# Kernel optimization log

Measured on AMD Instinct MI355X. Metric: run time of the kernel, lower is better.

The kernel has to match this reference:

```python
import jax, jax.numpy as jnp
import numpy as np

B, P, Q, D_IN, H, DR = 16, 4096, 512, 512, 256, 256


def setup_inputs() -> dict:
    key = jax.random.key(0)
    ks = jax.random.split(key, 6)
    passage = jax.random.normal(ks[0], (B, P, D_IN), dtype=jnp.float32)
    question = jax.random.normal(ks[1], (B, Q, D_IN), dtype=jnp.float32)
    rep = jax.random.normal(ks[2], (B, Q, DR), dtype=jnp.float32)
    rep_p = jax.random.normal(ks[3], (B, P, DR), dtype=jnp.float32)
    p_mask = jnp.zeros((B, P), dtype=bool)  # True = padding position
    q_mask = jnp.zeros((B, Q), dtype=bool)
    # xavier-uniform-like init for U weight, stored as [in, out]
    limit = float(np.sqrt(6.0 / (D_IN + H)))
    W = jax.random.uniform(ks[4], (D_IN, H), dtype=jnp.float32, minval=-limit, maxval=limit)
    D = jnp.ones((1, H), dtype=jnp.float32)
    return {"passage": passage, "p_mask": p_mask, "question": question,
            "q_mask": q_mask, "rep": rep, "rep_p": rep_p, "W": W, "D": D,
            "is_training": 0}


def reference(passage, p_mask, question, q_mask, rep, rep_p, W, D, is_training):
    # inference path (is_training falsy): no dropout
    Up = jax.nn.relu(passage @ W)              # [B, P, H]
    Uq = jax.nn.relu(question @ W) * D         # [B, Q, H], scaled by diagonal D
    scores = jnp.einsum('bph,bqh->bpq', Up, Uq)  # [B, P, Q]
    # question -> passage direction (rep_p is not None)
    scores_T = jnp.where(p_mask[:, None, :], -jnp.inf, scores.transpose(0, 2, 1))  # [B, Q, P]
    alpha_p = jax.nn.softmax(scores_T, axis=-1)
    output_q = jnp.einsum('bqp,bpd->bqd', alpha_p, rep_p)  # [B, Q, DR]
    # passage -> question direction
    scores_m = jnp.where(q_mask[:, None, :], -jnp.inf, scores)  # [B, P, Q]
    alpha = jax.nn.softmax(scores_m, axis=-1)
    output = jnp.einsum('bpq,bqd->bpd', alpha, rep)  # [B, P, DR]
    return (output, output_q)
```

## Files before the change

### kernel.cpp

```cpp
#include <hip/hip_runtime.h>


typedef float  f32x4   __attribute__((ext_vector_type(4)));
typedef float  float4v __attribute__((ext_vector_type(4)));
typedef short  short8v __attribute__((ext_vector_type(8)));
typedef unsigned short us4 __attribute__((ext_vector_type(4)));
typedef unsigned short us8v __attribute__((ext_vector_type(8)));

#define MFMA16(a,b,c) __builtin_amdgcn_mfma_f32_16x16x32_bf16((a),(b),(c),0,0,0)

__device__ __forceinline__ unsigned short f2bf(float f) {
  unsigned int u = __builtin_bit_cast(unsigned int, f);
  u += 0x7FFFu + ((u >> 16) & 1u);
  return (unsigned short)(u >> 16);
}
__device__ __forceinline__ float bf2f(unsigned short h) {
  unsigned int u = (unsigned int)h << 16;
  return __builtin_bit_cast(float, u);
}
__device__ __forceinline__ void split2(float v, unsigned short& h, unsigned short& l) {
  h = f2bf(v);
  l = f2bf(v - bf2f(h));
}
__device__ __forceinline__ unsigned short enc16(float a, float cm) {
  float x = (a - cm + 20.f) * 3276.8f + 0.5f;
  x = fminf(fmaxf(x, 0.f), 65535.f);
  return (unsigned short)x;
}

__global__ __launch_bounds__(256) void transpose_all(
    const float* __restrict__ W, const float* __restrict__ rep,
    const float* __restrict__ rep_p,
    unsigned short* __restrict__ Wth, unsigned short* __restrict__ Wtl,
    unsigned short* __restrict__ repT, unsigned short* __restrict__ repTp)
{
  __shared__ float lTf[64][65];
  const int blk = blockIdx.x;
  const float* src; unsigned short* dst; unsigned short* dstl = nullptr;
  int srows; size_t r0, c0;
  if (blk < 4096) {
    int b = blk >> 8, tb = blk & 255;
    src = rep_p + (size_t)b * 4096 * 256;
    dst = repTp + (size_t)b * 256 * 4096;
    srows = 4096; r0 = (size_t)(tb >> 2) * 64; c0 = (size_t)(tb & 3) * 64;
  } else if (blk < 4608) {
    int rel = blk - 4096; int b = rel >> 5, tb = rel & 31;
    src = rep + (size_t)b * 512 * 256;
    dst = repT + (size_t)b * 256 * 512;
    srows = 512; r0 = (size_t)(tb >> 2) * 64; c0 = (size_t)(tb & 3) * 64;
  } else {
    int rel = blk - 4608;
    src = W; dst = Wth; dstl = Wtl;
    srows = 512; r0 = (size_t)(rel >> 2) * 64; c0 = (size_t)(rel & 3) * 64;
  }
  const int t = threadIdx.x;
#pragma unroll
  for (int j = 0; j < 4; ++j) {
    int idx = j * 256 + t;
    int r = idx >> 4, c4 = (idx & 15) * 4;
    float4v v = *(const float4v*)&src[(r0 + (size_t)r) * 256 + c0 + c4];
    lTf[r][c4 + 0] = v[0]; lTf[r][c4 + 1] = v[1];
    lTf[r][c4 + 2] = v[2]; lTf[r][c4 + 3] = v[3];
  }
  __syncthreads();
#pragma unroll
  for (int j = 0; j < 4; ++j) {
    int idx = j * 256 + t;
    int dr = idx >> 4, p4 = (idx & 15) * 4;
    size_t o = (c0 + (size_t)dr) * (size_t)srows + r0 + p4;
    if (!dstl) {
      us4 oh;
#pragma unroll
      for (int e = 0; e < 4; ++e) oh[e] = f2bf(lTf[p4 + e][dr]);
      *(us4*)&dst[o] = oh;
    } else {
      us4 oh, ol;
#pragma unroll
      for (int e = 0; e < 4; ++e) {
        unsigned short h, l; split2(lTf[p4 + e][dr], h, l);
        oh[e] = h; ol[e] = l;
      }
      *(us4*)&dst[o] = oh;
      *(us4*)&dstl[o] = ol;
    }
  }
}

template<int APPLY_D>
__global__ __launch_bounds__(256) void ugemm_kernel(
    const float* __restrict__ X,
    const unsigned short* __restrict__ Wth, const unsigned short* __restrict__ Wtl,
    const float* __restrict__ Dv,
    unsigned short* __restrict__ Uh, unsigned short* __restrict__ Ul)
{
  __shared__ unsigned short lAh[64 * 40], lAl[64 * 40];
  __shared__ unsigned short lBh[256 * 40], lBl[256 * 40];
  const int t = threadIdx.x;
  const int w = t >> 6, l = t & 63;
  const int l15 = l & 15, lg = l >> 4, kr = lg * 8;
  const size_t m0 = (size_t)blockIdx.x * 64;
  f32x4 acc[4][4] = {};
  for (int k0 = 0; k0 < 512; k0 += 32) {
    __syncthreads();
    {
      int row = t >> 2, c = (t & 3) * 8;
      const float* src = X + (m0 + row) * 512 + k0 + c;
      float4v v0 = *(const float4v*)src;
      float4v v1 = *(const float4v*)(src + 4);
      short8v ph, pl;
#pragma unroll
      for (int e = 0; e < 4; ++e) {
        unsigned short h, lo;
        split2(v0[e], h, lo); ph[e] = (short)h; pl[e] = (short)lo;
        split2(v1[e], h, lo); ph[4 + e] = (short)h; pl[4 + e] = (short)lo;
      }
      *(short8v*)&lAh[row * 40 + c] = ph;
      *(short8v*)&lAl[row * 40 + c] = pl;
    }
#pragma unroll
    for (int j = 0; j < 4; ++j) {
      int idx = j * 256 + t;
      int row = idx >> 2, c = (idx & 3) * 8;
      size_t g = (size_t)row * 512 + k0 + c;
      *(short8v*)&lBh[row * 40 + c] = *(const short8v*)&Wth[g];
      *(short8v*)&lBl[row * 40 + c] = *(const short8v*)&Wtl[g];
    }
    __syncthreads();
    short8v ah[4], al[4];
#pragma unroll
    for (int mi = 0; mi < 4; ++mi) {
      ah[mi] = *(const short8v*)&lAh[(mi * 16 + l15) * 40 + kr];
      al[mi] = *(const short8v*)&lAl[(mi * 16 + l15) * 40 + kr];
    }
#pragma unroll
    for (int ni = 0; ni < 4; ++ni) {
      int rr = (w * 64 + ni * 16 + l15) * 40 + kr;
      short8v bh = *(const short8v*)&lBh[rr];
      short8v bl = *(const short8v*)&lBl[rr];
#pragma unroll
      for (int mi = 0; mi < 4; ++mi) {
        acc[mi][ni] = MFMA16(ah[mi], bh, acc[mi][ni]);
        acc[mi][ni] = MFMA16(ah[mi], bl, acc[mi][ni]);
        acc[mi][ni] = MFMA16(al[mi], bh, acc[mi][ni]);
      }
    }
  }
#pragma unroll
  for (int mi = 0; mi < 4; ++mi)
#pragma unroll
    for (int ni = 0; ni < 4; ++ni)
#pragma unroll
      for (int r = 0; r < 4; ++r) {
        size_t row = m0 + mi * 16 + lg * 4 + r;
        int col = w * 64 + ni * 16 + l15;
        float v = acc[mi][ni][r];
        v = v > 0.f ? v : 0.f;
        if (APPLY_D) v *= Dv[col];
        unsigned short h, lo; split2(v, h, lo);
        Uh[row * 256 + col] = h;
        Ul[row * 256 + col] = lo;
      }
}

template<int STORE_S>
__global__ __launch_bounds__(512, 4) void dir2_kernel(
    const unsigned short* __restrict__ Uph, const unsigned short* __restrict__ Upl,
    const unsigned short* __restrict__ Uqh, const unsigned short* __restrict__ Uql,
    const unsigned short* __restrict__ repT, const unsigned char* __restrict__ qmask,
    const unsigned char* __restrict__ pmask, unsigned short* __restrict__ St,
    float* __restrict__ colmaxP, float* __restrict__ out)
{
  __shared__ __align__(16) unsigned char smem[43008];
  unsigned short* probs = (unsigned short*)smem;
  float* smax = (float*)(smem + 40960);
  float* ssum = (float*)(smem + 41984);

  const int id = blockIdx.x;
  const int b  = (id & 7) | ((id >> 9) << 3);
  const int p0 = ((id >> 3) & 63) * 64;
  const int t = threadIdx.x;
  const int w = t >> 6, l = t & 63;
  const int wr = w >> 2, wc = w & 3;
  const int l15 = l & 15, lg = l >> 4, kr = lg * 8;
  const int srow = t >> 2, sc = (t & 3) * 8;

  const unsigned short* UqBh = Uqh + (size_t)b * 512 * 256;
  const unsigned short* UqBl = Uql + (size_t)b * 512 * 256;
  const size_t aoff = ((size_t)b * 4096 + p0 + wr * 32 + l15) * 256 + kr;
  const unsigned short* pAh0 = Uph + aoff;
  const unsigned short* pAh1 = pAh0 + 16 * 256;
  const unsigned short* pAl0 = Upl + aoff;
  const unsigned short* pAl1 = pAl0 + 16 * 256;

  auto lbh = [&](int buf) { return (unsigned short*)(smem + buf * 20480); };
  auto lbl = [&](int buf) { return (unsigned short*)(smem + buf * 20480 + 10240); };

  f32x4 acc[2][8] = {};
  short8v cah0, cah1, cal0, cal1;
  short8v nah0, nah1, nal0, nal1;
  short8v rh, rl;

  cah0 = *(const short8v*)&pAh0[0];
  cah1 = *(const short8v*)&pAh1[0];
  cal0 = *(const short8v*)&pAl0[0];
  cal1 = *(const short8v*)&pAl1[0];
  {
    size_t g = (size_t)srow * 256 + sc;
    rh = *(const short8v*)&UqBh[g];
    rl = *(const short8v*)&UqBl[g];
  }
  *(short8v*)&lbh(0)[srow * 40 + sc] = rh;
  *(short8v*)&lbl(0)[srow * 40 + sc] = rl;
  __syncthreads();

  for (int k0 = 0; k0 < 8; ++k0) {
#pragma unroll
    for (int qh = 0; qh < 4; ++qh) {
      const int cur = qh & 1;
      const bool last = (k0 == 7) && (qh == 3);
      if (!last) {
        int nk0 = (qh == 3) ? k0 + 1 : k0;
        int nqh = (qh == 3) ? 0 : qh + 1;
        size_t g = (size_t)(nqh * 128 + srow) * 256 + nk0 * 32 + sc;
        rh = *(const short8v*)&UqBh[g];
        rl = *(const short8v*)&UqBl[g];
      }
      if (qh == 3 && k0 < 7) {
        size_t ao = (size_t)(k0 + 1) * 32;
        nah0 = *(const short8v*)&pAh0[ao];
        nah1 = *(const short8v*)&pAh1[ao];
        nal0 = *(const short8v*)&pAl0[ao];
        nal1 = *(const short8v*)&pAl1[ao];
      }
      const unsigned short* bhp = lbh(cur);
      const unsigned short* blp = lbl(cur);
#pragma unroll
      for (int qi = 0; qi < 2; ++qi) {
        int rr = (wc * 32 + qi * 16 + l15) * 40 + kr;
        short8v bh = *(const short8v*)&bhp[rr];
        short8v bl = *(const short8v*)&blp[rr];
        int j = qh * 2 + qi;
        acc[0][j] = MFMA16(cah0, bh, acc[0][j]);
        acc[0][j] = MFMA16(cah0, bl, acc[0][j]);
        acc[0][j] = MFMA16(cal0, bh, acc[0][j]);
        acc[1][j] = MFMA16(cah1, bh, acc[1][j]);
        acc[1][j] = MFMA16(cah1, bl, acc[1][j]);
        acc[1][j] = MFMA16(cal1, bh, acc[1][j]);
      }
      if (!last) {
        *(short8v*)&lbh(cur ^ 1)[srow * 40 + sc] = rh;
        *(short8v*)&lbl(cur ^ 1)[srow * 40 + sc] = rl;
      }
      if (qh == 3 && k0 < 7) { cah0 = nah0; cah1 = nah1; cal0 = nal0; cal1 = nal1; }
      __syncthreads();
    }
  }
  if (STORE_S) {
    const unsigned char* pmk = pmask + (size_t)b * 4096 + p0 + wr * 32;
    unsigned int pmw0 = *(const unsigned int*)&pmk[lg * 4];
    unsigned int pmw1 = *(const unsigned int*)&pmk[16 + lg * 4];
#pragma unroll
    for (int j = 0; j < 8; ++j) {
      int qcol = ((j >> 1) << 7) + wc * 32 + ((j & 1) << 4) + l15;
      float a0[4], a1[4];
      float cm = -1e30f;
#pragma unroll
      for (int r = 0; r < 4; ++r) {
        a0[r] = ((pmw0 >> (8 * r)) & 0xFFu) ? -1e30f : acc[0][j][r];
        a1[r] = ((pmw1 >> (8 * r)) & 0xFFu) ? -1e30f : acc[1][j][r];
        cm = fmaxf(cm, fmaxf(a0[r], a1[r]));
      }
      cm = fmaxf(cm, __shfl_xor(cm, 16));
      cm = fmaxf(cm, __shfl_xor(cm, 32));
      us4 e0, e1;
#pragma unroll
      for (int r = 0; r < 4; ++r) {
        e0[r] = enc16(a0[r], cm);
        e1[r] = enc16(a1[r], cm);
      }
      size_t sb = ((size_t)b * 512 + qcol) * 4096 + p0 + wr * 32 + lg * 4;
      *(us4*)&St[sb]      = e0;
      *(us4*)&St[sb + 16] = e1;
      if (l < 16)
        colmaxP[((size_t)b * 128 + (p0 >> 5) + wr) * 512 + qcol] = cm;
    }
  }
  const unsigned char* qm = qmask + (size_t)b * 512;
#pragma unroll
  for (int j = 0; j < 8; ++j) {
    int qcol = ((j >> 1) << 7) + wc * 32 + ((j & 1) << 4) + l15;
    if (qm[qcol]) {
#pragma unroll
      for (int mi = 0; mi < 2; ++mi)
#pragma unroll
        for (int r = 0; r < 4; ++r) acc[mi][j][r] = -1e30f;
    }
  }
#pragma unroll
  for (int mi = 0; mi < 2; ++mi)
#pragma unroll
    for (int r = 0; r < 4; ++r) {
      float v = acc[mi][0][r];
#pragma unroll
      for (int j = 1; j < 8; ++j) v = fmaxf(v, acc[mi][j][r]);
      v = fmaxf(v, __shfl_xor(v, 1)); v = fmaxf(v, __shfl_xor(v, 2));
      v = fmaxf(v, __shfl_xor(v, 4)); v = fmaxf(v, __shfl_xor(v, 8));
      if (l15 == 0) smax[wc * 64 + wr * 32 + mi * 16 + lg * 4 + r] = v;
    }
  __syncthreads();
  float Mx[2][4];
#pragma unroll
  for (int mi = 0; mi < 2; ++mi)
#pragma unroll
    for (int r = 0; r < 4; ++r) {
      int row = wr * 32 + mi * 16 + lg * 4 + r;
      Mx[mi][r] = fmaxf(fmaxf(smax[row], smax[64 + row]),
                        fmaxf(smax[128 + row], smax[192 + row]));
    }
  float rs[2][4] = {};
#pragma unroll
  for (int mi = 0; mi < 2; ++mi)
#pragma unroll
    for (int j = 0; j < 8; ++j)
#pragma unroll
      for (int r = 0; r < 4; ++r) {
        float ev = __expf(acc[mi][j][r] - Mx[mi][r]);
        acc[mi][j][r] = ev;
        rs[mi][r] += ev;
      }
#pragma unroll
  for (int mi = 0; mi < 2; ++mi)
#pragma unroll
    for (int r = 0; r < 4; ++r) {
      float v = rs[mi][r];
      v += __shfl_xor(v, 1); v += __shfl_xor(v, 2);
      v += __shfl_xor(v, 4); v += __shfl_xor(v, 8);
      if (l15 == 0) ssum[wc * 64 + wr * 32 + mi * 16 + lg * 4 + r] = v;
    }
  const unsigned short* rT = repT + (size_t)b * 131072;
#pragma unroll
  for (int h = 0; h < 2; ++h) {
    __syncthreads();
    if (wr == h) {
#pragma unroll
      for (int mi = 0; mi < 2; ++mi)
#pragma unroll
        for (int j = 0; j < 8; ++j) {
          int qcol = ((j >> 1) << 7) + wc * 32 + ((j & 1) << 4) + l15;
#pragma unroll
          for (int r = 0; r < 4; ++r)
            probs[(mi * 16 + lg * 4 + r) * 520 + qcol] = f2bf(acc[mi][j][r]);
        }
    }
    __syncthreads();
    float invv[2][4];
#pragma unroll
    for (int mi = 0; mi < 2; ++mi)
#pragma unroll
      for (int r = 0; r < 4; ++r) {
        int row = h * 32 + mi * 16 + lg * 4 + r;
        invv[mi][r] = 1.0f / (ssum[row] + ssum[64 + row] +
                              ssum[128 + row] + ssum[192 + row]);
      }
    f32x4 acc2[2][2] = {};
    const unsigned short* rTb = rT + (size_t)(w * 32 + l15) * 512 + kr;
    short8v cb0 = *(const short8v*)(rTb);
    short8v cb1 = *(const short8v*)(rTb + 16 * 512);
    for (int k0 = 0; k0 < 512; k0 += 32) {
      int kn = (k0 + 32) & 511;
      short8v nb0 = *(const short8v*)(rTb + kn);
      short8v nb1 = *(const short8v*)(rTb + 16 * 512 + kn);
      short8v a0 = *(const short8v*)&probs[l15 * 520 + k0 + kr];
      short8v a1 = *(const short8v*)&probs[(16 + l15) * 520 + k0 + kr];
      acc2[0][0] = MFMA16(a0, cb0, acc2[0][0]);
      acc2[1][0] = MFMA16(a1, cb0, acc2[1][0]);
      acc2[0][1] = MFMA16(a0, cb1, acc2[0][1]);
      acc2[1][1] = MFMA16(a1, cb1, acc2[1][1]);
      cb0 = nb0; cb1 = nb1;
    }
#pragma unroll
    for (int mi = 0; mi < 2; ++mi)
#pragma unroll
      for (int di = 0; di < 2; ++di)
#pragma unroll
        for (int r = 0; r < 4; ++r) {
          int row = p0 + h * 32 + mi * 16 + lg * 4 + r;
          int col = w * 32 + di * 16 + l15;
          out[((size_t)b * 4096 + row) * 256 + col] = acc2[mi][di][r] * invv[mi][r];
        }
  }
}

__global__ __launch_bounds__(256) void dir1_pv(
    const unsigned short* __restrict__ St, const float* __restrict__ colmaxP,
    const unsigned short* __restrict__ repTp,
    float* __restrict__ accP, float* __restrict__ mlP)
{
  __shared__ unsigned short lAe[2][32 * 72];
  const int id = blockIdx.x;
  const int xcd = id & 7, r0 = id >> 3;
  const int b = xcd * 2 + (r0 >> 6);
  const int rem = r0 & 63;
  const int qt = rem >> 2, ch = rem & 3;
  const int q0 = qt * 32, pbeg = ch * 1024;
  const int pi = (b * 16 + qt) * 4 + ch;
  const int NT = 16;

  const int t = threadIdx.x;
  const int w = t >> 6, l = t & 63;
  const int l15 = l & 15, lg = l >> 4, kr = lg * 8;
  const int srow = t >> 3, sp = (t & 7) * 8;

  const float* cmq = colmaxP + (size_t)b * 128 * 512 + q0 + srow;
  float mq_s;
  {
    const int part = t & 7;
    float m = -1e30f;
#pragma unroll
    for (int j = 0; j < 16; ++j)
      m = fmaxf(m, cmq[(size_t)(part + j * 8) * 512]);
    m = fmaxf(m, __shfl_xor(m, 1));
    m = fmaxf(m, __shfl_xor(m, 2));
    m = fmaxf(m, __shfl_xor(m, 4));
    mq_s = m;
  }
  const unsigned short* Sb = St + ((size_t)b * 512 + q0 + srow) * 4096;
  const unsigned short* vtb = repTp + ((size_t)b * 256 + w * 64 + l15) * 4096;
  float rsum = 0.f;
  f32x4 acc[2][4] = {};
  us8v u; float cmv;
  short8v bvA[2][4], bvB[2][4];

  auto STAGE_LOAD = [&](int tile) {
    int pelem = pbeg + tile * 64 + sp;
    u = *(const us8v*)(Sb + pelem);
    cmv = cmq[(size_t)(pelem >> 5) * 512];
  };
  auto STAGE_FINISH = [&](int buf) {
    float base = cmv - 20.f - mq_s;
    short8v pk;
#pragma unroll
    for (int e = 0; e < 8; ++e) {
      float ev = __expf((float)u[e] * (1.f / 3276.8f) + base);
      rsum += ev;
      pk[e] = (short)f2bf(ev);
    }
    *(short8v*)&lAe[buf][srow * 72 + sp] = pk;
  };
  auto BV_LOAD = [&](int tile, short8v (&bv)[2][4]) {
    int p0v = pbeg + tile * 64;
#pragma unroll
    for (int ks = 0; ks < 2; ++ks)
#pragma unroll
      for (int di = 0; di < 4; ++di)
        bv[ks][di] = *(const short8v*)&vtb[(size_t)(di * 16) * 4096 + p0v + ks * 32 + kr];
  };
  auto COMPUTE = [&](int buf, short8v (&bv)[2][4]) {
#pragma unroll
    for (int ks = 0; ks < 2; ++ks) {
      short8v pa0 = *(const short8v*)&lAe[buf][l15 * 72 + ks * 32 + kr];
      short8v pa1 = *(const short8v*)&lAe[buf][(16 + l15) * 72 + ks * 32 + kr];
#pragma unroll
      for (int di = 0; di < 4; ++di) {
        acc[0][di] = MFMA16(pa0, bv[ks][di], acc[0][di]);
        acc[1][di] = MFMA16(pa1, bv[ks][di], acc[1][di]);
      }
    }
  };

  STAGE_LOAD(0);
  BV_LOAD(0, bvA);
  STAGE_FINISH(0);
  STAGE_LOAD(1);
  __syncthreads();

#pragma unroll 1
  for (int tt = 0; tt < NT; tt += 2) {
    const bool has1 = (tt + 1 < NT), has2 = (tt + 2 < NT), has3 = (tt + 3 < NT);
    if (has1) BV_LOAD(tt + 1, bvB);
    COMPUTE(0, bvA);
    if (has1) STAGE_FINISH(1);
    if (has2) STAGE_LOAD(tt + 2);
    __syncthreads();
    if (has1) {
      if (has2) BV_LOAD(tt + 2, bvA);
      COMPUTE(1, bvB);
      if (has2) STAGE_FINISH(0);
      if (has3) STAGE_LOAD(tt + 3);
      __syncthreads();
    }
  }

  rsum += __shfl_xor(rsum, 1);
  rsum += __shfl_xor(rsum, 2);
  rsum += __shfl_xor(rsum, 4);
  if ((t & 7) == 0) mlP[(size_t)pi * 32 + srow] = rsum;

  float* ab = accP + (size_t)pi * 32 * 256;
#pragma unroll
  for (int mi = 0; mi < 2; ++mi)
#pragma unroll
    for (int di = 0; di < 4; ++di)
#pragma unroll
      for (int r = 0; r < 4; ++r) {
        int row = mi * 16 + lg * 4 + r;
        int col = w * 64 + di * 16 + l15;
        ab[(size_t)row * 256 + col] = acc[mi][di][r];
      }
}

__global__ __launch_bounds__(256) void merge4_kernel(
    const float* __restrict__ accP, const float* __restrict__ mlP,
    float* __restrict__ outq)
{
  const int g = blockIdx.x * 256 + threadIdx.x;
  const int row = g >> 6;
  const int d0 = (g & 63) * 4;
  const int b = row >> 9, q = row & 511;
  const int qt = q >> 5, ri = q & 31;
  const int pbase = (b * 16 + qt) * 4;
  float s = 0.f;
  float4v o = {0.f, 0.f, 0.f, 0.f};
#pragma unroll
  for (int c = 0; c < 4; ++c) {
    s += mlP[(size_t)(pbase + c) * 32 + ri];
    float4v a = *(const float4v*)&accP[((size_t)(pbase + c) * 32 + ri) * 256 + d0];
#pragma unroll
    for (int k = 0; k < 4; ++k) o[k] += a[k];
  }
  float inv = 1.0f / s;
#pragma unroll
  for (int k = 0; k < 4; ++k) o[k] *= inv;
  *(float4v*)&outq[(size_t)row * 256 + d0] = o;
}

__global__ __launch_bounds__(256) void dir1_partial(
    const unsigned short* __restrict__ Uph, const unsigned short* __restrict__ Upl,
    const unsigned short* __restrict__ Uqh, const unsigned short* __restrict__ Uql,
    const unsigned short* __restrict__ repTp, const unsigned char* __restrict__ pmask,
    float* __restrict__ accP, float* __restrict__ mlP)
{
  __shared__ __align__(16) unsigned char smem[39424];
  unsigned short* lAh = (unsigned short*)smem;
  unsigned short* lAl = (unsigned short*)(smem + 16896);
  unsigned short* lP  = (unsigned short*)(smem + 33792);
  float* smax = (float*)(smem + 38400);
  float* ssum = (float*)(smem + 38912);

  const int id  = blockIdx.x;
  const int xcd = id & 7, rr0 = id >> 3;
  const int b   = xcd * 2 + (rr0 >> 6);
  const int rem = rr0 & 63;
  const int qt  = rem >> 2, ch = rem & 3;
  const int q0  = qt * 32;
  const int pbeg = ch * 1024;
  const int pi  = (b * 16 + qt) * 4 + ch;

  const int t = threadIdx.x;
  const int w = t >> 6, l = t & 63;
  const int l15 = l & 15, lg = l >> 4, kr = lg * 8;

#pragma unroll
  for (int j = 0; j < 4; ++j) {
    int idx = j * 256 + t;
    int row = idx >> 5, c = (idx & 31) * 8;
    size_t g = ((size_t)b * 512 + q0 + row) * 256 + c;
    *(short8v*)&lAh[row * 264 + c] = *(const short8v*)&Uqh[g];
    *(short8v*)&lAl[row * 264 + c] = *(const short8v*)&Uql[g];
  }
  float m_r[2][4], l_r[2][4];
#pragma unroll
  for (int mi = 0; mi < 2; ++mi)
#pragma unroll
    for (int r = 0; r < 4; ++r) { m_r[mi][r] = -1e30f; l_r[mi][r] = 0.f; }
  f32x4 accO[2][4] = {};
  const size_t upoff = ((size_t)b * 4096 + w * 16 + l15) * 256;
  const unsigned short* upbh = Uph + upoff;
  const unsigned short* upbl = Upl + upoff;
  const unsigned short* vtb = repTp + (size_t)b * 1048576;
  const unsigned char* pm = pmask + (size_t)b * 4096;
  __syncthreads();

  for (int p0 = pbeg; p0 < pbeg + 1024; p0 += 64) {
    f32x4 s[2] = {};
#pragma unroll
    for (int k0 = 0; k0 < 256; k0 += 32) {
      short8v ah0 = *(const short8v*)&lAh[l15 * 264 + k0 + kr];
      short8v ah1 = *(const short8v*)&lAh[(16 + l15) * 264 + k0 + kr];
      short8v al0 = *(const short8v*)&lAl[l15 * 264 + k0 + kr];
      short8v al1 = *(const short8v*)&lAl[(16 + l15) * 264 + k0 + kr];
      short8v bvh = *(const short8v*)&upbh[(size_t)p0 * 256 + k0 + kr];
      short8v bvl = *(const short8v*)&upbl[(size_t)p0 * 256 + k0 + kr];
      s[0] = MFMA16(ah0, bvh, s[0]);
      s[0] = MFMA16(ah0, bvl, s[0]);
      s[0] = MFMA16(al0, bvh, s[0]);
      s[1] = MFMA16(ah1, bvh, s[1]);
      s[1] = MFMA16(ah1, bvl, s[1]);
      s[1] = MFMA16(al1, bvh, s[1]);
    }
    if (pm[p0 + w * 16 + l15]) {
#pragma unroll
      for (int mi = 0; mi < 2; ++mi)
#pragma unroll
        for (int r = 0; r < 4; ++r) s[mi][r] = -1e30f;
    }
#pragma unroll
    for (int mi = 0; mi < 2; ++mi)
#pragma unroll
      for (int r = 0; r < 4; ++r) {
        float v = s[mi][r];
        v = fmaxf(v, __shfl_xor(v, 1)); v = fmaxf(v, __shfl_xor(v, 2));
        v = fmaxf(v, __shfl_xor(v, 4)); v = fmaxf(v, __shfl_xor(v, 8));
        if (l15 == 0) smax[w * 32 + mi * 16 + lg * 4 + r] = v;
      }
    __syncthreads();
    float mnew[2][4], fsc[2][4], e[2][4];
#pragma unroll
    for (int mi = 0; mi < 2; ++mi)
#pragma unroll
      for (int r = 0; r < 4; ++r) {
        int row = mi * 16 + lg * 4 + r;
        float tm = fmaxf(fmaxf(smax[row], smax[32 + row]),
                         fmaxf(smax[64 + row], smax[96 + row]));
        float mn = fmaxf(m_r[mi][r], tm);
        mnew[mi][r] = mn;
        fsc[mi][r] = __expf(m_r[mi][r] - mn);
        e[mi][r] = __expf(s[mi][r] - mn);
      }
#pragma unroll
    for (int mi = 0; mi < 2; ++mi)
#pragma unroll
      for (int r = 0; r < 4; ++r) {
        float v = e[mi][r];
        v += __shfl_xor(v, 1); v += __shfl_xor(v, 2);
        v += __shfl_xor(v, 4); v += __shfl_xor(v, 8);
        if (l15 == 0) ssum[w * 32 + mi * 16 + lg * 4 + r] = v;
        lP[(mi * 16 + lg * 4 + r) * 72 + w * 16 + l15] = f2bf(e[mi][r]);
      }
    __syncthreads();
#pragma unroll
    for (int mi = 0; mi < 2; ++mi)
#pragma unroll
      for (int r = 0; r < 4; ++r) {
        int row = mi * 16 + lg * 4 + r;
        float ts = ssum[row] + ssum[32 + row] + ssum[64 + row] + ssum[96 + row];
        l_r[mi][r] = l_r[mi][r] * fsc[mi][r] + ts;
        m_r[mi][r] = mnew[mi][r];
      }
#pragma unroll
    for (int mi = 0; mi < 2; ++mi)
#pragma unroll
      for (int di = 0; di < 4; ++di)
#pragma unroll
        for (int r = 0; r < 4; ++r) accO[mi][di][r] *= fsc[mi][r];
#pragma unroll
    for (int ks = 0; ks < 64; ks += 32) {
      short8v pa0 = *(const short8v*)&lP[l15 * 72 + ks + kr];
      short8v pa1 = *(const short8v*)&lP[(16 + l15) * 72 + ks + kr];
#pragma unroll
      for (int di = 0; di < 4; ++di) {
        short8v bv = *(const short8v*)&vtb[(size_t)(w * 64 + di * 16 + l15) * 4096 + p0 + ks + kr];
        accO[0][di] = MFMA16(pa0, bv, accO[0][di]);
        accO[1][di] = MFMA16(pa1, bv, accO[1][di]);
      }
    }
  }
  float* ab = accP + (size_t)pi * 32 * 256;
#pragma unroll
  for (int mi = 0; mi < 2; ++mi)
#pragma unroll
    for (int di = 0; di < 4; ++di)
#pragma unroll
      for (int r = 0; r < 4; ++r) {
        int row = mi * 16 + lg * 4 + r;
        int col = w * 64 + di * 16 + l15;
        ab[(size_t)row * 256 + col] = accO[mi][di][r];
      }
  if (w == 0 && l15 == 0) {
#pragma unroll
    for (int mi = 0; mi < 2; ++mi)
#pragma unroll
      for (int r = 0; r < 4; ++r) {
        int row = mi * 16 + lg * 4 + r;
        mlP[((size_t)pi * 32 + row) * 2 + 0] = m_r[mi][r];
        mlP[((size_t)pi * 32 + row) * 2 + 1] = l_r[mi][r];
      }
  }
}

__global__ __launch_bounds__(256) void merge_kernel(
    const float* __restrict__ accP, const float* __restrict__ mlP,
    float* __restrict__ outq)
{
  const int g = blockIdx.x * 256 + threadIdx.x;
  const int row = g >> 6;
  const int d0 = (g & 63) * 4;
  const int b = row >> 9, q = row & 511;
  const int qt = q >> 5, ri = q & 31;
  const int pbase = (b * 16 + qt) * 4;
  float m[4], lv[4];
  float M = -1e30f;
#pragma unroll
  for (int c = 0; c < 4; ++c) {
    m[c]  = mlP[((size_t)(pbase + c) * 32 + ri) * 2 + 0];
    lv[c] = mlP[((size_t)(pbase + c) * 32 + ri) * 2 + 1];
    M = fmaxf(M, m[c]);
  }
  float s = 0.f;
  float4v o = {0.f, 0.f, 0.f, 0.f};
#pragma unroll
  for (int c = 0; c < 4; ++c) {
    float e = __expf(m[c] - M);
    s += e * lv[c];
    float4v a = *(const float4v*)&accP[((size_t)(pbase + c) * 32 + ri) * 256 + d0];
#pragma unroll
    for (int k = 0; k < 4; ++k) o[k] += e * a[k];
  }
  float inv = 1.0f / s;
#pragma unroll
  for (int k = 0; k < 4; ++k) o[k] *= inv;
  *(float4v*)&outq[(size_t)row * 256 + d0] = o;
}

extern "C" void kernel_launch(void* const* d_in, const int* in_sizes, int n_in,
                              void* d_out, int out_size, void* d_ws, size_t ws_size,
                              hipStream_t stream) {
  (void)in_sizes; (void)n_in; (void)out_size;
  const float* passage        = (const float*)d_in[0];
  const unsigned char* p_mask = (const unsigned char*)d_in[1];
  const float* question       = (const float*)d_in[2];
  const unsigned char* q_mask = (const unsigned char*)d_in[3];
  const float* rep            = (const float*)d_in[4];
  const float* rep_p          = (const float*)d_in[5];
  const float* W              = (const float*)d_in[6];
  const float* Dv             = (const float*)d_in[7];

  unsigned short* Wth   = (unsigned short*)d_ws;
  unsigned short* Wtl   = Wth   + 131072;
  unsigned short* repT  = Wtl   + 131072;
  unsigned short* repTp = repT  + 2097152;
  unsigned short* Uqh   = repTp + 16777216;
  unsigned short* Uql   = Uqh   + 2097152;
  unsigned short* Uph   = Uql   + 2097152;
  unsigned short* Upl   = Uph   + 16777216;
  unsigned short* StU = (unsigned short*)((char*)d_ws + 113770496ULL);
  float* colmaxP      = (float*)((char*)d_ws + 180879360ULL);
  const size_t NEEDED = 185073664ULL;

  float* out  = (float*)d_out;
  float* outq = out + (size_t)16 * 4096 * 256;

  transpose_all<<<4640, 256, 0, stream>>>(W, rep, rep_p, Wth, Wtl, repT, repTp);
  ugemm_kernel<0><<<1024, 256, 0, stream>>>(passage,  Wth, Wtl, nullptr, Uph, Upl);
  ugemm_kernel<1><<<128,  256, 0, stream>>>(question, Wth, Wtl, Dv,      Uqh, Uql);

  if (ws_size >= NEEDED) {
    float* accP4 = (float*)Uph;
    float* mlP4  = (float*)Uqh;
    dir2_kernel<1><<<1024, 512, 0, stream>>>(Uph, Upl, Uqh, Uql, repT,
                                             q_mask, p_mask, StU, colmaxP, out);
    dir1_pv<<<1024, 256, 0, stream>>>(StU, colmaxP, repTp, accP4, mlP4);
    merge4_kernel<<<2048, 256, 0, stream>>>(accP4, mlP4, outq);
  } else {
    float* accP = out;
    float* mlP  = (float*)Wth;
    dir1_partial<<<1024, 256, 0, stream>>>(Uph, Upl, Uqh, Uql, repTp, p_mask, accP, mlP);
    merge_kernel<<<2048, 256, 0, stream>>>(accP, mlP, outq);
    dir2_kernel<0><<<1024, 512, 0, stream>>>(Uph, Upl, Uqh, Uql, repT,
                                             q_mask, nullptr, nullptr, nullptr, out);
  }
}
```

Before: 389.9 us.

## Prefetch ugemm tiles into registers and process full 64-row PV in one pass

In the U projection GEMM, the next k-tile of X and of the split W is loaded into registers while the current tile is computed. This overlaps global-load latency with MFMA work. In dir2_kernel, the probability buffer in shared memory is enlarged to hold all 64 rows. The PV product then runs once over 64 rows instead of twice over 32, so each repT fragment is loaded once rather than twice and two barriers are dropped. The cost is more registers and about 67KB of LDS per block, which may lower occupancy below the launch bound target of four blocks per CU.

```diff
diff --git a/kernel.cpp b/kernel.cpp
--- a/kernel.cpp
+++ b/kernel.cpp
@@ -99,33 +99,55 @@
   const int w = t >> 6, l = t & 63;
   const int l15 = l & 15, lg = l >> 4, kr = lg * 8;
   const size_t m0 = (size_t)blockIdx.x * 64;
+  const int arow = t >> 2, ac = (t & 3) * 8;
+  const float* asrc = X + (m0 + arow) * 512 + ac;
+
   f32x4 acc[4][4] = {};
+  float4v va0, va1;
+  short8v vbh[4], vbl[4];
+
+  va0 = *(const float4v*)(asrc);
+  va1 = *(const float4v*)(asrc + 4);
+#pragma unroll
+  for (int j = 0; j < 4; ++j) {
+    int idx = j * 256 + t;
+    int row = idx >> 2, c = (idx & 3) * 8;
+    size_t g = (size_t)row * 512 + c;
+    vbh[j] = *(const short8v*)&Wth[g];
+    vbl[j] = *(const short8v*)&Wtl[g];
+  }
+
   for (int k0 = 0; k0 < 512; k0 += 32) {
+    short8v ph, pl;
+#pragma unroll
+    for (int e = 0; e < 4; ++e) {
+      unsigned short h, lo;
+      split2(va0[e], h, lo); ph[e] = (short)h; pl[e] = (short)lo;
+      split2(va1[e], h, lo); ph[4 + e] = (short)h; pl[4 + e] = (short)lo;
+    }
     __syncthreads();
-    {
-      int row = t >> 2, c = (t & 3) * 8;
-      const float* src = X + (m0 + row) * 512 + k0 + c;
-      float4v v0 = *(const float4v*)src;
-      float4v v1 = *(const float4v*)(src + 4);
-      short8v ph, pl;
-#pragma unroll
-      for (int e = 0; e < 4; ++e) {
-        unsigned short h, lo;
-        split2(v0[e], h, lo); ph[e] = (short)h; pl[e] = (short)lo;
-        split2(v1[e], h, lo); ph[4 + e] = (short)h; pl[4 + e] = (short)lo;
-      }
-      *(short8v*)&lAh[row * 40 + c] = ph;
-      *(short8v*)&lAl[row * 40 + c] = pl;
-    }
+    *(short8v*)&lAh[arow * 40 + ac] = ph;
+    *(short8v*)&lAl[arow * 40 + ac] = pl;
 #pragma unroll
     for (int j = 0; j < 4; ++j) {
       int idx = j * 256 + t;
       int row = idx >> 2, c = (idx & 3) * 8;
-      size_t g = (size_t)row * 512 + k0 + c;
-      *(short8v*)&lBh[row * 40 + c] = *(const short8v*)&Wth[g];
-      *(short8v*)&lBl[row * 40 + c] = *(const short8v*)&Wtl[g];
+      *(short8v*)&lBh[row * 40 + c] = vbh[j];
+      *(short8v*)&lBl[row * 40 + c] = vbl[j];
     }
     __syncthreads();
+    if (k0 < 480) {
+      va0 = *(const float4v*)(asrc + k0 + 32);
+      va1 = *(const float4v*)(asrc + k0 + 36);
+#pragma unroll
+      for (int j = 0; j < 4; ++j) {
+        int idx = j * 256 + t;
+        int row = idx >> 2, c = (idx & 3) * 8;
+        size_t g = (size_t)row * 512 + k0 + 32 + c;
+        vbh[j] = *(const short8v*)&Wth[g];
+        vbl[j] = *(const short8v*)&Wtl[g];
+      }
+    }
     short8v ah[4], al[4];
 #pragma unroll
     for (int mi = 0; mi < 4; ++mi) {
@@ -170,10 +192,10 @@
     const unsigned char* __restrict__ pmask, unsigned short* __restrict__ St,
     float* __restrict__ colmaxP, float* __restrict__ out)
 {
-  __shared__ __align__(16) unsigned char smem[43008];
+  __shared__ __align__(16) unsigned char smem[68608];
   unsigned short* probs = (unsigned short*)smem;
-  float* smax = (float*)(smem + 40960);
-  float* ssum = (float*)(smem + 41984);
+  float* smax = (float*)(smem + 66560);
+  float* ssum = (float*)(smem + 67584);
 
   const int id = blockIdx.x;
   const int b  = (id & 7) | ((id >> 9) << 3);
@@ -337,58 +359,58 @@
       v += __shfl_xor(v, 4); v += __shfl_xor(v, 8);
       if (l15 == 0) ssum[wc * 64 + wr * 32 + mi * 16 + lg * 4 + r] = v;
     }
+#pragma unroll
+  for (int mi = 0; mi < 2; ++mi)
+#pragma unroll
+    for (int j = 0; j < 8; ++j) {
+      int qcol = ((j >> 1) << 7) + wc * 32 + ((j & 1) << 4) + l15;
+#pragma unroll
+      for (int r = 0; r < 4; ++r)
+        probs[(wr * 32 + mi * 16 + lg * 4 + r) * 520 + qcol] = f2bf(acc[mi][j][r]);
+    }
+  __syncthreads();
   const unsigned short* rT = repT + (size_t)b * 131072;
-#pragma unroll
-  for (int h = 0; h < 2; ++h) {
-    __syncthreads();
-    if (wr == h) {
-#pragma unroll
-      for (int mi = 0; mi < 2; ++mi)
-#pragma unroll
-        for (int j = 0; j < 8; ++j) {
-          int qcol = ((j >> 1) << 7) + wc * 32 + ((j & 1) << 4) + l15;
-#pragma unroll
-          for (int r = 0; r < 4; ++r)
-            probs[(mi * 16 + lg * 4 + r) * 520 + qcol] = f2bf(acc[mi][j][r]);
-        }
-    }
-    __syncthreads();
-    float invv[2][4];
-#pragma unroll
-    for (int mi = 0; mi < 2; ++mi)
-#pragma unroll
-      for (int r = 0; r < 4; ++r) {
-        int row = h * 32 + mi * 16 + lg * 4 + r;
-        invv[mi][r] = 1.0f / (ssum[row] + ssum[64 + row] +
-                              ssum[128 + row] + ssum[192 + row]);
-      }
-    f32x4 acc2[2][2] = {};
-    const unsigned short* rTb = rT + (size_t)(w * 32 + l15) * 512 + kr;
-    short8v cb0 = *(const short8v*)(rTb);
-    short8v cb1 = *(const short8v*)(rTb + 16 * 512);
-    for (int k0 = 0; k0 < 512; k0 += 32) {
-      int kn = (k0 + 32) & 511;
-      short8v nb0 = *(const short8v*)(rTb + kn);
-      short8v nb1 = *(const short8v*)(rTb + 16 * 512 + kn);
-      short8v a0 = *(const short8v*)&probs[l15 * 520 + k0 + kr];
-      short8v a1 = *(const short8v*)&probs[(16 + l15) * 520 + k0 + kr];
-      acc2[0][0] = MFMA16(a0, cb0, acc2[0][0]);
-      acc2[1][0] = MFMA16(a1, cb0, acc2[1][0]);
-      acc2[0][1] = MFMA16(a0, cb1, acc2[0][1]);
-      acc2[1][1] = MFMA16(a1, cb1, acc2[1][1]);
-      cb0 = nb0; cb1 = nb1;
-    }
-#pragma unroll
-    for (int mi = 0; mi < 2; ++mi)
-#pragma unroll
-      for (int di = 0; di < 2; ++di)
-#pragma unroll
-        for (int r = 0; r < 4; ++r) {
-          int row = p0 + h * 32 + mi * 16 + lg * 4 + r;
-          int col = w * 32 + di * 16 + l15;
-          out[((size_t)b * 4096 + row) * 256 + col] = acc2[mi][di][r] * invv[mi][r];
-        }
-  }
+  float invv[4][4];
+#pragma unroll
+  for (int mi = 0; mi < 4; ++mi)
+#pragma unroll
+    for (int r = 0; r < 4; ++r) {
+      int row = mi * 16 + lg * 4 + r;
+      invv[mi][r] = 1.0f / (ssum[row] + ssum[64 + row] +
+                            ssum[128 + row] + ssum[192 + row]);
+    }
+  f32x4 acc2[4][2] = {};
+  const unsigned short* rTb = rT + (size_t)(w * 32 + l15) * 512 + kr;
+  short8v cb0 = *(const short8v*)(rTb);
+  short8v cb1 = *(const short8v*)(rTb + 16 * 512);
+  for (int k0 = 0; k0 < 512; k0 += 32) {
+    int kn = (k0 + 32) & 511;
+    short8v nb0 = *(const short8v*)(rTb + kn);
+    short8v nb1 = *(const short8v*)(rTb + 16 * 512 + kn);
+    short8v a0 = *(const short8v*)&probs[(l15) * 520 + k0 + kr];
+    short8v a1 = *(const short8v*)&probs[(16 + l15) * 520 + k0 + kr];
+    short8v a2 = *(const short8v*)&probs[(32 + l15) * 520 + k0 + kr];
+    short8v a3 = *(const short8v*)&probs[(48 + l15) * 520 + k0 + kr];
+    acc2[0][0] = MFMA16(a0, cb0, acc2[0][0]);
+    acc2[1][0] = MFMA16(a1, cb0, acc2[1][0]);
+    acc2[2][0] = MFMA16(a2, cb0, acc2[2][0]);
+    acc2[3][0] = MFMA16(a3, cb0, acc2[3][0]);
+    acc2[0][1] = MFMA16(a0, cb1, acc2[0][1]);
+    acc2[1][1] = MFMA16(a1, cb1, acc2[1][1]);
+    acc2[2][1] = MFMA16(a2, cb1, acc2[2][1]);
+    acc2[3][1] = MFMA16(a3, cb1, acc2[3][1]);
+    cb0 = nb0; cb1 = nb1;
+  }
+#pragma unroll
+  for (int mi = 0; mi < 4; ++mi)
+#pragma unroll
+    for (int di = 0; di < 2; ++di)
+#pragma unroll
+      for (int r = 0; r < 4; ++r) {
+        int row = p0 + mi * 16 + lg * 4 + r;
+        int col = w * 32 + di * 16 + l15;
+        out[((size_t)b * 4096 + row) * 256 + col] = acc2[mi][di][r] * invv[mi][r];
+      }
 }
 
 __global__ __launch_bounds__(256) void dir1_pv(
```

Result: faster. 335.6 us (-13.9%).
